# Kernel optimization log

Hardware: AMD Instinct MI355X
Metric: run time of the kernel (lower is better)

## Reference

```python
import jax, jax.numpy as jnp
import numpy as np

B, S, I, H = 64, 512, 1024, 1024

def setup_inputs() -> dict:
    key = jax.random.key(0)
    k1, k2, k3 = jax.random.split(key, 3)
    scale = 1.0 / np.sqrt(I + H)
    x = jax.random.normal(k1, (B, S, I), dtype=jnp.float32)
    # Stacked gate weights, order: [cell_candidate, forget, update, output]
    W = jax.random.normal(k2, (4 * H, I + H), dtype=jnp.float32) * scale
    b = jax.random.normal(k3, (4 * H,), dtype=jnp.float32) * scale
    return {"x": x, "W": W, "b": b}

def _lstm(x, W, b):
    Wx = W[:, :I]   # (4H, I)
    Wh = W[:, I:]   # (4H, H)
    # Precompute input contribution for all timesteps in one big GEMM
    xW = jnp.einsum('bsi,gi->bsg', x, Wx) + b  # (B, S, 4H)
    xW_t = jnp.transpose(xW, (1, 0, 2))        # (S, B, 4H)

    def step(carry, xw):
        h, c = carry
        pre = xw + h @ Wh.T                    # (B, 4H)
        cand, f, u, o = jnp.split(pre, 4, axis=-1)
        cand = jnp.tanh(cand)
        f = jax.nn.sigmoid(f)
        u = jax.nn.sigmoid(u)
        o = jax.nn.sigmoid(o)
        c = u * cand + f * c
        h = o * jnp.tanh(c)
        return (h, c), h

    h0 = jnp.zeros((x.shape[0], H), dtype=x.dtype)
    c0 = jnp.zeros((x.shape[0], H), dtype=x.dtype)
    (h_n, c_n), outs = jax.lax.scan(step, (h0, c0), xW_t)
    output_seq = jnp.transpose(outs, (1, 0, 2))  # (B, S, H)
    return output_seq, h_n[None], c_n[None]

def reference(x, W, b):
    return _lstm(x, W, b)
```

## Files before the change

kernel.cpp:

```cpp
#include <hip/hip_runtime.h>
#include <math.h>

typedef unsigned short ushort_t;
typedef unsigned long long u64;
typedef __attribute__((ext_vector_type(4))) float f32x4;
typedef __attribute__((ext_vector_type(8))) short s16x8;
typedef __attribute__((ext_vector_type(4))) int s32x4;

#define XW_OFF   0UL
#define XB_OFF   268435456UL
#define WXP_OFF  335544320UL
#define WHP_OFF  343932928UL
#define BP_OFF   352321536UL
#define HBUF_OFF 352337920UL
#define CNT_OFF  352600064UL

__device__ __forceinline__ ushort_t f2bf(float f) {
  unsigned u = __builtin_bit_cast(unsigned, f);
  unsigned r = u + 0x7FFFu + ((u >> 16) & 1u);
  return (ushort_t)(r >> 16);
}
__device__ __forceinline__ float bf2f(ushort_t h) {
  unsigned u = ((unsigned)h) << 16;
  return __builtin_bit_cast(float, u);
}
__device__ __forceinline__ float sigm(float x) { return 1.f / (1.f + __expf(-x)); }
__device__ __forceinline__ float tanh_f(float x) {
  float t = __expf(-2.f * fabsf(x));
  float r = (1.f - t) / (1.f + t);
  return x >= 0.f ? r : -r;
}
__device__ __forceinline__ void gload_lds16(const void* g, void* l) {
  __builtin_amdgcn_global_load_lds(
      (const __attribute__((address_space(1))) unsigned int*)g,
      (__attribute__((address_space(3))) unsigned int*)l, 16, 0, 0);
}
__device__ __forceinline__ void gload16_cc(const void* p, s32x4& v) {
  asm volatile("global_load_dwordx4 %0, %1, off sc1"
               : "=v"(v) : "v"(p) : "memory");
}

__global__ __launch_bounds__(256) void convert_x(const float* __restrict__ x,
                                                 ushort_t* __restrict__ xb) {
  long gid = (long)blockIdx.x * 256 + threadIdx.x;
  const float4* x4 = (const float4*)x;
  float4 f0 = x4[gid * 2];
  float4 f1 = x4[gid * 2 + 1];
  s16x8 o;
  o[0] = (short)f2bf(f0.x); o[1] = (short)f2bf(f0.y);
  o[2] = (short)f2bf(f0.z); o[3] = (short)f2bf(f0.w);
  o[4] = (short)f2bf(f1.x); o[5] = (short)f2bf(f1.y);
  o[6] = (short)f2bf(f1.z); o[7] = (short)f2bf(f1.w);
  ((s16x8*)xb)[gid] = o;
}

__global__ __launch_bounds__(256) void prep_pack(const float* __restrict__ W,
                                                 const float* __restrict__ bias,
                                                 ushort_t* __restrict__ wxp,
                                                 ushort_t* __restrict__ whp,
                                                 float* __restrict__ bp,
                                                 ushort_t* __restrict__ hbuf,
                                                 int* __restrict__ cnt) {
  long gid = (long)blockIdx.x * 256 + threadIdx.x;
  if (gid < 524288) {
    int l = gid & 63, kc = (int)((gid >> 6) & 31), w = (int)((gid >> 11) & 3);
    int kb = (int)(gid >> 13);
    int li = l & 15, quad = l >> 4;
    int colb = w * 16 + li;
    int G = (colb & 3) * 1024 + kb * 16 + (colb >> 2);
    int kk = kc * 32 + quad * 8;
    const float* src = W + (long)G * 2048 + 1024 + kk;
    ushort_t* dst = whp + gid * 8;
#pragma unroll
    for (int j = 0; j < 8; ++j) dst[j] = f2bf(src[j]);
  } else if (gid < 1048576) {
    long id = gid - 524288;
    int k8 = (int)(id & 127);
    int R = (int)(id >> 7);
    int c = R & 63, kb = R >> 6;
    int G = (c & 3) * 1024 + kb * 16 + (c >> 2);
    const float* src = W + (long)G * 2048 + k8 * 8;
    ushort_t* dst = wxp + (long)R * 1024 + k8 * 8;
#pragma unroll
    for (int j = 0; j < 8; ++j) dst[j] = f2bf(src[j]);
  } else if (gid < 1048576 + 4096) {
    int R = (int)(gid - 1048576);
    int c = R & 63, kb = R >> 6;
    int G = (c & 3) * 1024 + kb * 16 + (c >> 2);
    bp[R] = bias[G];
  } else if (gid < 1048576 + 4096 + 8192) {
    long id = gid - 1048576 - 4096;
    s16x8 z = {0, 0, 0, 0, 0, 0, 0, 0};
    ((s16x8*)hbuf)[id] = z;
  } else if (gid < 1048576 + 4096 + 8192 + 2048) {
    cnt[gid - 1048576 - 4096 - 8192] = 0;
  }
}

__global__ __launch_bounds__(256) void lstm_phase1(const ushort_t* __restrict__ xb,
                                                   const ushort_t* __restrict__ wxp,
                                                   const float* __restrict__ bp,
                                                   ushort_t* __restrict__ xw) {
  __shared__ ushort_t As[16 * 512];
  __shared__ ushort_t Bs[16 * 512];
  int bid = blockIdx.x;
  int nt = bid & 31, mtb = bid >> 5;
  int n0 = nt * 128;
  int t0 = mtb * 2;
  int tid = threadIdx.x, w = tid >> 6, l = tid & 63;
  int quad = l >> 4, li = l & 15;
  int mh = w & 1, nh = w >> 1;
  f32x4 acc[4][4] = {};

  for (int k0 = 0; k0 < 1024; k0 += 64) {
    __syncthreads();
#pragma unroll
    for (int i = 0; i < 4; ++i) {
      int c = w * 4 + i;
      int mt = c >> 1, kcl = c & 1;
      int r = mt * 16 + li;
      int tt = t0 + (r >> 6), bb = r & 63;
      gload_lds16(xb + (long)(bb * 512 + tt) * 1024 + k0 + kcl * 32 + quad * 8,
                  &As[c * 512]);
      int rn = n0 + mt * 16 + li;
      gload_lds16(wxp + (long)rn * 1024 + k0 + kcl * 32 + quad * 8, &Bs[c * 512]);
    }
    __syncthreads();
#pragma unroll
    for (int kcl = 0; kcl < 2; ++kcl) {
      s16x8 av[4], bv[4];
#pragma unroll
      for (int i = 0; i < 4; ++i)
        av[i] = *(const s16x8*)&As[((mh * 4 + i) * 2 + kcl) * 512 + l * 8];
#pragma unroll
      for (int j = 0; j < 4; ++j)
        bv[j] = *(const s16x8*)&Bs[((nh * 4 + j) * 2 + kcl) * 512 + l * 8];
#pragma unroll
      for (int i = 0; i < 4; ++i)
#pragma unroll
        for (int j = 0; j < 4; ++j)
          acc[i][j] =
              __builtin_amdgcn_mfma_f32_16x16x32_bf16(av[i], bv[j], acc[i][j], 0, 0, 0);
    }
  }
#pragma unroll
  for (int j = 0; j < 4; ++j) {
    float bj = bp[n0 + nh * 64 + j * 16 + li];
#pragma unroll
    for (int i = 0; i < 4; ++i) {
#pragma unroll
      for (int r = 0; r < 4; ++r) {
        int lr = mh * 64 + i * 16 + quad * 4 + r;
        long off = ((long)mtb * 128 + lr) * 4096 + (n0 + nh * 64 + j * 16 + li);
        xw[off] = f2bf(acc[i][j][r] + bj);
      }
    }
  }
}

__global__ __launch_bounds__(256) void lstm_phase2(const ushort_t* __restrict__ xw,
                                                   const ushort_t* __restrict__ whp,
                                                   ushort_t* __restrict__ hbuf,
                                                   float* __restrict__ out,
                                                   int* __restrict__ counters) {
  __shared__ ushort_t Aimg[32 * 512];
  int bid = blockIdx.x;
  int gr = bid >> 6, kb = bid & 63;
  int tid = threadIdx.x, w = tid >> 6, l = tid & 63;
  int quad = l >> 4, li = l & 15;
  int colb = w * 16 + li;
  int gg = colb & 3;
  int jj = colb >> 2;
  int colh = kb * 16 + jj;

  int* flags = counters + gr * 256;

  s16x8 bfr[32];
  const ushort_t* wp = whp + (long)(kb * 4 + w) * 32 * 512 + l * 8;
#pragma unroll
  for (int kc = 0; kc < 32; ++kc) bfr[kc] = *(const s16x8*)(wp + kc * 512);

  float cst[4] = {0.f, 0.f, 0.f, 0.f};
  ushort_t pf[4];
#pragma unroll
  for (int r = 0; r < 4; ++r)
    pf[r] = xw[(long)(gr * 16 + quad * 4 + r) * 4096 + kb * 64 + colb];

  int base = l & ~3;

  for (int t = 0; t < 512; ++t) {
    int p = t & 1;
    if (t > 0) {
      const void* fl4 = (const void*)(flags + l * 4);
      int g = 0;
      for (;;) {
        s32x4 f;
        asm volatile("global_load_dwordx4 %0, %1, off sc1\n\ts_waitcnt vmcnt(0)"
                     : "=v"(f) : "v"(fl4) : "memory");
        if (__all(f[0] >= t && f[1] >= t && f[2] >= t && f[3] >= t)) break;
        if (++g > 1024) break;
      }
    }
    const char* hsrc = (const char*)hbuf + (long)p * 131072 + (long)gr * 32768;
    s32x4 hv[8];
#pragma unroll
    for (int ci = 0; ci < 8; ++ci) {
      int kc = w * 8 + ci;
      gload16_cc(hsrc + li * 2048 + kc * 64 + quad * 16, hv[ci]);
    }
    f32x4 a0, a1, a2, a3;
#pragma unroll
    for (int r = 0; r < 4; ++r) a0[r] = bf2f(pf[r]);
    a1 = (f32x4)0.f; a2 = (f32x4)0.f; a3 = (f32x4)0.f;
    if (t < 511) {
#pragma unroll
      for (int r = 0; r < 4; ++r)
        pf[r] = xw[(long)((t + 1) * 64 + gr * 16 + quad * 4 + r) * 4096 + kb * 64 + colb];
    }
    asm volatile("s_waitcnt vmcnt(0)" ::: "memory");
    __builtin_amdgcn_sched_barrier(0);
#pragma unroll
    for (int ci = 0; ci < 8; ++ci) {
      int kc = w * 8 + ci;
      *(s32x4*)&Aimg[kc * 512 + l * 8] = hv[ci];
    }
    __syncthreads();
#pragma unroll
    for (int kc = 0; kc < 32; ++kc) {
      s16x8 a = *(const s16x8*)&Aimg[kc * 512 + l * 8];
      switch (kc & 3) {
        case 0: a0 = __builtin_amdgcn_mfma_f32_16x16x32_bf16(a, bfr[kc], a0, 0, 0, 0); break;
        case 1: a1 = __builtin_amdgcn_mfma_f32_16x16x32_bf16(a, bfr[kc], a1, 0, 0, 0); break;
        case 2: a2 = __builtin_amdgcn_mfma_f32_16x16x32_bf16(a, bfr[kc], a2, 0, 0, 0); break;
        default: a3 = __builtin_amdgcn_mfma_f32_16x16x32_bf16(a, bfr[kc], a3, 0, 0, 0); break;
      }
    }
    f32x4 pre4 = (a0 + a1) + (a2 + a3);

    float hn[4], cn[4];
#pragma unroll
    for (int r = 0; r < 4; ++r) {
      float pre = pre4[r];
      float candp = __shfl(pre, base + 0, 64);
      float fp_ = __shfl(pre, base + 1, 64);
      float up = __shfl(pre, base + 2, 64);
      float op = __shfl(pre, base + 3, 64);
      float c_ = sigm(up) * tanh_f(candp) + sigm(fp_) * cst[r];
      cst[r] = c_;
      cn[r] = c_;
      hn[r] = sigm(op) * tanh_f(c_);
    }
    ushort_t* hdst = hbuf + (p ^ 1) * 65536;
#pragma unroll
    for (int r = 0; r < 4; ++r) {
      unsigned hb = (unsigned)f2bf(hn[r]);
      unsigned c0 = __shfl(hb, base - (l & 3) - (li & 12) + 0, 64);
      unsigned c1 = __shfl(hb, (quad << 4) + 4, 64);
      unsigned c2 = __shfl(hb, (quad << 4) + 8, 64);
      unsigned c3 = __shfl(hb, (quad << 4) + 12, 64);
      c0 = __shfl(hb, (quad << 4) + 0, 64);
      if (li == 0) {
        int b = gr * 16 + quad * 4 + r;
        u64 packed = (u64)c0 | ((u64)c1 << 16) | ((u64)c2 << 32) | ((u64)c3 << 48);
        __hip_atomic_store((u64*)&hdst[b * 1024 + kb * 16 + w * 4], packed,
                           __ATOMIC_RELAXED, __HIP_MEMORY_SCOPE_AGENT);
      }
    }
    asm volatile("s_waitcnt vmcnt(0)" ::: "memory");
    if (l == 0)
      __hip_atomic_store(flags + kb * 4 + w, t + 1, __ATOMIC_RELAXED,
                         __HIP_MEMORY_SCOPE_AGENT);
    if (gg == 0) {
#pragma unroll
      for (int r = 0; r < 4; ++r) {
        int b = gr * 16 + quad * 4 + r;
        out[((long)b * 512 + t) * 1024 + colh] = hn[r];
        if (t == 511) {
          out[33554432 + b * 1024 + colh] = hn[r];
          out[33619968 + b * 1024 + colh] = cn[r];
        }
      }
    }
  }
}

extern "C" void kernel_launch(void* const* d_in, const int* in_sizes, int n_in,
                              void* d_out, int out_size, void* d_ws, size_t ws_size,
                              hipStream_t stream) {
  const float* x = (const float*)d_in[0];
  const float* W = (const float*)d_in[1];
  const float* b = (const float*)d_in[2];
  float* out = (float*)d_out;
  char* ws = (char*)d_ws;
  ushort_t* xw = (ushort_t*)(ws + XW_OFF);
  ushort_t* xb = (ushort_t*)(ws + XB_OFF);
  ushort_t* wxp = (ushort_t*)(ws + WXP_OFF);
  ushort_t* whp = (ushort_t*)(ws + WHP_OFF);
  float* bp = (float*)(ws + BP_OFF);
  ushort_t* hbuf = (ushort_t*)(ws + HBUF_OFF);
  int* cnt = (int*)(ws + CNT_OFF);

  convert_x<<<16384, 256, 0, stream>>>(x, xb);
  prep_pack<<<4152, 256, 0, stream>>>(W, b, wxp, whp, bp, hbuf, cnt);
  lstm_phase1<<<8192, 256, 0, stream>>>(xb, wxp, bp, xw);
  lstm_phase2<<<256, 256, 0, stream>>>(xw, whp, hbuf, out, cnt);
}
```

Baseline: 4.566 ms.

## Replace per-step flag counters with timestep-tagged hidden-state words

The persistent recurrent kernel now writes each pair of bf16 hidden values together with the timestep number in one 64-bit atomic store. Consumers spin directly on the h data until every tag matches the current step. This removes the separate flag store, its store-drain wait, and the extra flag-polling round trip per step. In exchange it doubles the h traffic, needs a new zeroing kernel, and adds a second __syncthreads per step to protect the shared-memory staging buffer.

Result: faster. 4.462 ms (-2.3%).

```diff
diff --git a/kernel.cpp b/kernel.cpp
--- a/kernel.cpp
+++ b/kernel.cpp
@@ -97,6 +97,12 @@
   }
 }
 
+__global__ __launch_bounds__(256) void zero_hbuf2(s32x4* __restrict__ hb) {
+  long gid = (long)blockIdx.x * 256 + threadIdx.x;
+  s32x4 z = {0, 0, 0, 0};
+  hb[gid] = z;
+}
+
 __global__ __launch_bounds__(256) void lstm_phase1(const ushort_t* __restrict__ xb,
                                                    const ushort_t* __restrict__ wxp,
                                                    const float* __restrict__ bp,
@@ -160,9 +166,8 @@
 
 __global__ __launch_bounds__(256) void lstm_phase2(const ushort_t* __restrict__ xw,
                                                    const ushort_t* __restrict__ whp,
-                                                   ushort_t* __restrict__ hbuf,
-                                                   float* __restrict__ out,
-                                                   int* __restrict__ counters) {
+                                                   u64* __restrict__ hbuf2,
+                                                   float* __restrict__ out) {
   __shared__ ushort_t Aimg[32 * 512];
   int bid = blockIdx.x;
   int gr = bid >> 6, kb = bid & 63;
@@ -173,8 +178,6 @@
   int jj = colb >> 2;
   int colh = kb * 16 + jj;
 
-  int* flags = counters + gr * 256;
-
   s16x8 bfr[32];
   const ushort_t* wp = whp + (long)(kb * 4 + w) * 32 * 512 + l * 8;
 #pragma unroll
@@ -190,23 +193,26 @@
 
   for (int t = 0; t < 512; ++t) {
     int p = t & 1;
-    if (t > 0) {
-      const void* fl4 = (const void*)(flags + l * 4);
+    const char* hb = (const char*)hbuf2 + (long)p * 262144 + (long)(gr * 16 + li) * 4096;
+    s32x4 hv[16];
+    {
       int g = 0;
       for (;;) {
-        s32x4 f;
-        asm volatile("global_load_dwordx4 %0, %1, off sc1\n\ts_waitcnt vmcnt(0)"
-                     : "=v"(f) : "v"(fl4) : "memory");
-        if (__all(f[0] >= t && f[1] >= t && f[2] >= t && f[3] >= t)) break;
-        if (++g > 1024) break;
-      }
-    }
-    const char* hsrc = (const char*)hbuf + (long)p * 131072 + (long)gr * 32768;
-    s32x4 hv[8];
-#pragma unroll
-    for (int ci = 0; ci < 8; ++ci) {
-      int kc = w * 8 + ci;
-      gload16_cc(hsrc + li * 2048 + kc * 64 + quad * 16, hv[ci]);
+#pragma unroll
+        for (int ci = 0; ci < 8; ++ci) {
+          int kc = w * 8 + ci;
+          const char* a = hb + (kc * 16 + quad * 4) * 8;
+          gload16_cc(a, hv[2 * ci]);
+          gload16_cc(a + 16, hv[2 * ci + 1]);
+        }
+        asm volatile("s_waitcnt vmcnt(0)" ::: "memory");
+        __builtin_amdgcn_sched_barrier(0);
+        int ok = 1;
+#pragma unroll
+        for (int i = 0; i < 16; ++i) ok &= (hv[i][1] == t) & (hv[i][3] == t);
+        if (__all(ok)) break;
+        if (++g > 4096) break;
+      }
     }
     f32x4 a0, a1, a2, a3;
 #pragma unroll
@@ -217,12 +223,15 @@
       for (int r = 0; r < 4; ++r)
         pf[r] = xw[(long)((t + 1) * 64 + gr * 16 + quad * 4 + r) * 4096 + kb * 64 + colb];
     }
-    asm volatile("s_waitcnt vmcnt(0)" ::: "memory");
-    __builtin_amdgcn_sched_barrier(0);
 #pragma unroll
     for (int ci = 0; ci < 8; ++ci) {
       int kc = w * 8 + ci;
-      *(s32x4*)&Aimg[kc * 512 + l * 8] = hv[ci];
+      s32x4 d;
+      d[0] = hv[2 * ci][0];
+      d[1] = hv[2 * ci][2];
+      d[2] = hv[2 * ci + 1][0];
+      d[3] = hv[2 * ci + 1][2];
+      *(s32x4*)&Aimg[kc * 512 + l * 8] = d;
     }
     __syncthreads();
 #pragma unroll
@@ -236,6 +245,7 @@
       }
     }
     f32x4 pre4 = (a0 + a1) + (a2 + a3);
+    __syncthreads();
 
     float hn[4], cn[4];
 #pragma unroll
@@ -250,26 +260,25 @@
       cn[r] = c_;
       hn[r] = sigm(op) * tanh_f(c_);
     }
-    ushort_t* hdst = hbuf + (p ^ 1) * 65536;
+    u64* hd = hbuf2 + (long)(p ^ 1) * 32768;
+    u64 tag = ((u64)(unsigned)(t + 1)) << 32;
 #pragma unroll
     for (int r = 0; r < 4; ++r) {
-      unsigned hb = (unsigned)f2bf(hn[r]);
-      unsigned c0 = __shfl(hb, base - (l & 3) - (li & 12) + 0, 64);
-      unsigned c1 = __shfl(hb, (quad << 4) + 4, 64);
-      unsigned c2 = __shfl(hb, (quad << 4) + 8, 64);
-      unsigned c3 = __shfl(hb, (quad << 4) + 12, 64);
-      c0 = __shfl(hb, (quad << 4) + 0, 64);
+      unsigned hb_ = (unsigned)f2bf(hn[r]);
+      unsigned c0 = __shfl(hb_, (quad << 4) + 0, 64);
+      unsigned c1 = __shfl(hb_, (quad << 4) + 4, 64);
+      unsigned c2 = __shfl(hb_, (quad << 4) + 8, 64);
+      unsigned c3 = __shfl(hb_, (quad << 4) + 12, 64);
       if (li == 0) {
         int b = gr * 16 + quad * 4 + r;
-        u64 packed = (u64)c0 | ((u64)c1 << 16) | ((u64)c2 << 32) | ((u64)c3 << 48);
-        __hip_atomic_store((u64*)&hdst[b * 1024 + kb * 16 + w * 4], packed,
+        u64 tA = (u64)c0 | ((u64)c1 << 16) | tag;
+        u64 tB = (u64)c2 | ((u64)c3 << 16) | tag;
+        __hip_atomic_store(hd + (long)b * 512 + kb * 8 + w * 2, tA,
                            __ATOMIC_RELAXED, __HIP_MEMORY_SCOPE_AGENT);
-      }
-    }
-    asm volatile("s_waitcnt vmcnt(0)" ::: "memory");
-    if (l == 0)
-      __hip_atomic_store(flags + kb * 4 + w, t + 1, __ATOMIC_RELAXED,
-                         __HIP_MEMORY_SCOPE_AGENT);
+        __hip_atomic_store(hd + (long)b * 512 + kb * 8 + w * 2 + 1, tB,
+                           __ATOMIC_RELAXED, __HIP_MEMORY_SCOPE_AGENT);
+      }
+    }
     if (gg == 0) {
 #pragma unroll
       for (int r = 0; r < 4; ++r) {
@@ -299,9 +308,11 @@
   float* bp = (float*)(ws + BP_OFF);
   ushort_t* hbuf = (ushort_t*)(ws + HBUF_OFF);
   int* cnt = (int*)(ws + CNT_OFF);
+  u64* hbuf2 = (u64*)(ws + XB_OFF);
 
   convert_x<<<16384, 256, 0, stream>>>(x, xb);
   prep_pack<<<4152, 256, 0, stream>>>(W, b, wxp, whp, bp, hbuf, cnt);
   lstm_phase1<<<8192, 256, 0, stream>>>(xb, wxp, bp, xw);
-  lstm_phase2<<<256, 256, 0, stream>>>(xw, whp, hbuf, out, cnt);
-}
+  zero_hbuf2<<<128, 256, 0, stream>>>((s32x4*)hbuf2);
+  lstm_phase2<<<256, 256, 0, stream>>>(xw, whp, hbuf2, out);
+}
```
